# Kernel optimization log

Measured on AMD Instinct MI355X. Metric: run time of the kernel, lower is better.

## Reference

```python
import jax, jax.numpy as jnp
import numpy as np

HEADS = 16
D_MODEL = 1024
D_K = D_MODEL // HEADS


def setup_inputs() -> dict:
    key = jax.random.key(0)
    ks = jax.random.split(key, 11)
    B, S, D = 4, 2048, D_MODEL
    q = jax.random.normal(ks[0], (B, S, D), dtype=jnp.float32)
    k = jax.random.normal(ks[1], (B, S, D), dtype=jnp.float32)
    v = jax.random.normal(ks[2], (B, S, D), dtype=jnp.float32)
    s = 1.0 / np.sqrt(D)
    Wq = jax.random.normal(ks[3], (D, D), dtype=jnp.float32) * s
    bq = jax.random.normal(ks[4], (D,), dtype=jnp.float32) * 0.01
    Wk = jax.random.normal(ks[5], (D, D), dtype=jnp.float32) * s
    bk = jax.random.normal(ks[6], (D,), dtype=jnp.float32) * 0.01
    Wv = jax.random.normal(ks[7], (D, D), dtype=jnp.float32) * s
    bv = jax.random.normal(ks[8], (D,), dtype=jnp.float32) * 0.01
    Wo = jax.random.normal(ks[9], (D, D), dtype=jnp.float32) * s
    bo = jax.random.normal(ks[10], (D,), dtype=jnp.float32) * 0.01
    return {"q": q, "k": k, "v": v, "Wq": Wq, "bq": bq, "Wk": Wk, "bk": bk,
            "Wv": Wv, "bv": bv, "Wo": Wo, "bo": bo}


def reference(q, k, v, Wq, bq, Wk, bk, Wv, bv, Wo, bo):
    B, Sq, D = q.shape
    Sk = k.shape[1]
    # Linear projections (torch Linear: x @ W.T + b)
    q_ = (q @ Wq.T + bq).reshape(B, Sq, HEADS, D_K).transpose(0, 2, 1, 3)  # [B,H,Sq,Dk]
    k_ = (k @ Wk.T + bk).reshape(B, Sk, HEADS, D_K).transpose(0, 2, 1, 3)  # [B,H,Sk,Dk]
    v_ = (v @ Wv.T + bv).reshape(B, Sk, HEADS, D_K).transpose(0, 2, 1, 3)  # [B,H,Sk,Dk]
    scores = jnp.einsum("bhqd,bhkd->bhqk", q_, k_) / jnp.sqrt(jnp.float32(D_K))
    attn = jax.nn.softmax(scores, axis=-1)
    ctx = jnp.einsum("bhqk,bhkd->bhqd", attn, v_)  # [B,H,Sq,Dk]
    concat = ctx.transpose(0, 2, 1, 3).reshape(B, Sq, D)
    # dropout p=0 -> identity (eval)
    return concat @ Wo.T + bo
```

## Files before the change

kernel.cpp:

```cpp
#include <hip/hip_runtime.h>
#include <hip/hip_bf16.h>
#include <stdint.h>

typedef unsigned short u16;
typedef __attribute__((ext_vector_type(8))) short bf16x8;
typedef __attribute__((ext_vector_type(4))) float f32x4;
typedef __attribute__((ext_vector_type(16))) float f32x16;
typedef __attribute__((ext_vector_type(4))) int i32x4;
typedef __attribute__((ext_vector_type(4))) unsigned short us4;

#define BATCH 4
#define HEADS 16
#define SEQ   2048
#define DMODEL 1024
#define DK    64
#define QSCALE (0.125f * 1.44269504088896340736f)

__device__ __forceinline__ u16 f2bf(float f) {
  __hip_bfloat16 h = __float2bfloat16(f);
  return *reinterpret_cast<u16*>(&h);
}

__device__ __forceinline__ int cvtpk(float a, float b) {
  int r;
  asm("v_cvt_pk_bf16_f32 %0, %1, %2" : "=v"(r) : "v"(a), "v"(b));
  return r;
}

__device__ __forceinline__ void plswap(int& a, int& b) {
  asm volatile("v_permlane32_swap_b32 %0, %1" : "+v"(a), "+v"(b));
}

__device__ __forceinline__ void gload_lds16(const u16* g, u16* l) {
  __builtin_amdgcn_global_load_lds((const __attribute__((address_space(1))) void*)g,
                                   (__attribute__((address_space(3))) void*)l, 16, 0, 0);
}

__device__ __forceinline__ void cvt8(const float* __restrict__ in, u16* __restrict__ out, long i) {
  float4 a = *(const float4*)(in + i);
  float4 b = *(const float4*)(in + i + 4);
  i32x4 pk;
  pk[0] = cvtpk(a.x, a.y); pk[1] = cvtpk(a.z, a.w);
  pk[2] = cvtpk(b.x, b.y); pk[3] = cvtpk(b.z, b.w);
  *(i32x4*)(out + i) = pk;
}

__global__ void cvt_all(const float* __restrict__ q, const float* __restrict__ k,
                        const float* __restrict__ v, const float* __restrict__ w0,
                        const float* __restrict__ w1, const float* __restrict__ w2,
                        const float* __restrict__ w3, u16* __restrict__ qo,
                        u16* __restrict__ ko, u16* __restrict__ vo,
                        u16* __restrict__ o0, u16* __restrict__ o1,
                        u16* __restrict__ o2, u16* __restrict__ o3) {
  const int sel = blockIdx.y;
  long i = ((long)blockIdx.x * blockDim.x + threadIdx.x) * 8;
  if (sel >= 3 && i >= (long)DMODEL * DMODEL) return;
  const float* in = (sel == 0) ? q : (sel == 1) ? k : (sel == 2) ? v
                  : (sel == 3) ? w0 : (sel == 4) ? w1 : (sel == 5) ? w2 : w3;
  u16* out = (sel == 0) ? qo : (sel == 1) ? ko : (sel == 2) ? vo
           : (sel == 3) ? o0 : (sel == 4) ? o1 : (sel == 5) ? o2 : o3;
  cvt8(in, out, i);
}

__global__ __launch_bounds__(256)
void gemm_qkv(const u16* __restrict__ qb, const u16* __restrict__ kb,
              const u16* __restrict__ vb, const u16* __restrict__ Wqb,
              const u16* __restrict__ Wkb, const u16* __restrict__ Wvb,
              const float* __restrict__ bq, const float* __restrict__ bk,
              const float* __restrict__ bv, u16* __restrict__ Qp,
              u16* __restrict__ Kp, u16* __restrict__ Vt) {
  __shared__ u16 smem[128 * 64 * 2];
  u16* As = smem;
  u16* Bs = smem + 128 * 64;
  const int K = DMODEL;
  const int tid = threadIdx.x;
  const int lane = tid & 63;
  const int w = tid >> 6;
  const int wr = w >> 1, wc = w & 1;
  const int lr = lane & 15, lg = lane >> 4;

  const int wg = blockIdx.y * 24 + blockIdx.x;
  const int swz = (wg & 7) * (1536 >> 3) + (wg >> 3);
  const int bcolg = swz % 24;
  const int brow = swz / 24;
  const int sel = bcolg >> 3;
  const int bcol = bcolg & 7;

  const u16* A  = (sel == 0) ? qb : (sel == 1) ? kb : vb;
  const u16* Bm = (sel == 0) ? Wqb : (sel == 1) ? Wkb : Wvb;
  const float* bias = (sel == 0) ? bq : (sel == 1) ? bk : bv;

  const size_t aBase = (size_t)(brow * 128) * K;
  const size_t bBase = (size_t)(bcol * 128) * K;

  int srow[4], scol[4];
#pragma unroll
  for (int j = 0; j < 4; j++) {
    const int c = tid + j * 256;
    srow[j] = c >> 3;
    scol[j] = ((c & 7) ^ (srow[j] & 7)) * 8;
  }

  f32x4 acc[4][4] = {};

  for (int k0 = 0; k0 < K; k0 += 64) {
#pragma unroll
    for (int j = 0; j < 4; j++) {
      const int c = tid + j * 256;
      gload_lds16(A + aBase + (size_t)srow[j] * K + k0 + scol[j], As + c * 8);
      gload_lds16(Bm + bBase + (size_t)srow[j] * K + k0 + scol[j], Bs + c * 8);
    }
    __syncthreads();
#pragma unroll
    for (int h = 0; h < 2; h++) {
      bf16x8 a[4], b[4];
#pragma unroll
      for (int i = 0; i < 4; i++) {
        const int row = wr * 64 + i * 16 + lr;
        a[i] = *(const bf16x8*)&As[row * 64 + (((h * 4 + lg) ^ (row & 7)) * 8)];
      }
#pragma unroll
      for (int j = 0; j < 4; j++) {
        const int row = wc * 64 + j * 16 + lr;
        b[j] = *(const bf16x8*)&Bs[row * 64 + (((h * 4 + lg) ^ (row & 7)) * 8)];
      }
#pragma unroll
      for (int i = 0; i < 4; i++)
#pragma unroll
        for (int j = 0; j < 4; j++)
          acc[i][j] = __builtin_amdgcn_mfma_f32_16x16x32_bf16(a[i], b[j], acc[i][j], 0, 0, 0);
    }
    __syncthreads();
  }

  if (sel < 2) {
    u16* Cout = (sel == 0) ? Qp : Kp;
    const float oscale = (sel == 0) ? QSCALE : 1.f;
#pragma unroll
    for (int j = 0; j < 4; j++) {
      const int col = bcol * 128 + wc * 64 + j * 16 + lr;
      const float bv_ = bias[col];
#pragma unroll
      for (int i = 0; i < 4; i++) {
        const int row0 = brow * 128 + wr * 64 + i * 16 + lg * 4;
#pragma unroll
        for (int r = 0; r < 4; r++)
          Cout[(size_t)(row0 + r) * DMODEL + col] = f2bf((acc[i][j][r] + bv_) * oscale);
      }
    }
  } else {
    const int b = brow >> 4;
    const int s0 = (brow & 15) * 128;
#pragma unroll
    for (int j = 0; j < 4; j++) {
      const int col = wc * 64 + j * 16 + lr;
      const int xsw = (col & 7) << 3;
      const float bv_ = bias[bcol * 128 + col];
#pragma unroll
      for (int i = 0; i < 4; i++) {
        const int row0 = wr * 64 + i * 16 + lg * 4;
#pragma unroll
        for (int pr = 0; pr < 2; pr++) {
          float e0 = acc[i][j][pr * 2] + bv_;
          float e1 = acc[i][j][pr * 2 + 1] + bv_;
          *(int*)&smem[col * 128 + ((row0 + pr * 2) ^ xsw)] = cvtpk(e0, e1);
        }
      }
    }
    __syncthreads();
    const int col = tid >> 1, h2 = tid & 1;
    const int xsw = (col & 7) << 3;
    const int c = bcol * 128 + col;
    const int hh = c >> 6, dk = c & 63;
    u16* dst = Vt + (size_t)((b * 16 + hh) * 64 + dk) * SEQ + s0 + h2 * 64;
#pragma unroll
    for (int jj = 0; jj < 8; jj++) {
      bf16x8 vrow = *(const bf16x8*)&smem[col * 128 + ((h2 * 64 + jj * 8) ^ xsw)];
      *(bf16x8*)(dst + jj * 8) = vrow;
    }
  }
}

__global__ __launch_bounds__(256)
void gemm_bt(const u16* __restrict__ A, const u16* __restrict__ Bm,
             const float* __restrict__ bias, float* __restrict__ Cout,
             int M, int N, int K) {
  __shared__ u16 As[128 * 64];
  __shared__ u16 Bs[128 * 64];
  const int tid = threadIdx.x;
  const int lane = tid & 63;
  const int w = tid >> 6;
  const int wr = w >> 1, wc = w & 1;
  const int lr = lane & 15, lg = lane >> 4;

  const int nwg = gridDim.x * gridDim.y;
  const int wg = blockIdx.y * gridDim.x + blockIdx.x;
  const int swz = (wg & 7) * (nwg >> 3) + (wg >> 3);
  const int bcol = swz % gridDim.x;
  const int brow = swz / gridDim.x;

  const size_t aBase = (size_t)(brow * 128) * K;
  const size_t bBase = (size_t)(bcol * 128) * K;

  int srow[4], scol[4];
#pragma unroll
  for (int j = 0; j < 4; j++) {
    const int c = tid + j * 256;
    srow[j] = c >> 3;
    scol[j] = ((c & 7) ^ (srow[j] & 7)) * 8;
  }

  f32x4 acc[4][4] = {};

  for (int k0 = 0; k0 < K; k0 += 64) {
#pragma unroll
    for (int j = 0; j < 4; j++) {
      const int c = tid + j * 256;
      gload_lds16(A + aBase + (size_t)srow[j] * K + k0 + scol[j], As + c * 8);
      gload_lds16(Bm + bBase + (size_t)srow[j] * K + k0 + scol[j], Bs + c * 8);
    }
    __syncthreads();
#pragma unroll
    for (int h = 0; h < 2; h++) {
      bf16x8 a[4], b[4];
#pragma unroll
      for (int i = 0; i < 4; i++) {
        const int row = wr * 64 + i * 16 + lr;
        a[i] = *(const bf16x8*)&As[row * 64 + (((h * 4 + lg) ^ (row & 7)) * 8)];
      }
#pragma unroll
      for (int j = 0; j < 4; j++) {
        const int row = wc * 64 + j * 16 + lr;
        b[j] = *(const bf16x8*)&Bs[row * 64 + (((h * 4 + lg) ^ (row & 7)) * 8)];
      }
#pragma unroll
      for (int i = 0; i < 4; i++)
#pragma unroll
        for (int j = 0; j < 4; j++)
          acc[i][j] = __builtin_amdgcn_mfma_f32_16x16x32_bf16(a[i], b[j], acc[i][j], 0, 0, 0);
    }
    __syncthreads();
  }

#pragma unroll
  for (int j = 0; j < 4; j++) {
    const int col = bcol * 128 + wc * 64 + j * 16 + lr;
    const float bv = bias[col];
#pragma unroll
    for (int i = 0; i < 4; i++) {
      const int row0 = brow * 128 + wr * 64 + i * 16 + lg * 4;
#pragma unroll
      for (int r = 0; r < 4; r++)
        Cout[(size_t)(row0 + r) * N + col] = acc[i][j][r] + bv;
    }
  }
}

__device__ __forceinline__ void pack_group(const float* p, int* pw) {
  int W0 = cvtpk(p[0], p[1]);
  int W1 = cvtpk(p[2], p[3]);
  int W2 = cvtpk(p[4], p[5]);
  int W3 = cvtpk(p[6], p[7]);
  plswap(W0, W2);
  plswap(W1, W3);
  pw[0] = W0; pw[1] = W1; pw[2] = W2; pw[3] = W3;
}

__global__ __launch_bounds__(256, 4)
void attn2(const u16* __restrict__ Qp, const u16* __restrict__ Kp,
           const u16* __restrict__ Vt, u16* __restrict__ ctx) {
  __shared__ __align__(16) u16 smem[16384];
  const int tid = threadIdx.x;
  const int lane = tid & 63, w = tid >> 6;
  const int hi = lane >> 5;
  const int l31 = lane & 31;
  const int bh = blockIdx.y;
  const int b = bh >> 4, h = bh & 15;
  const int q0 = blockIdx.x * 128 + w * 32;

  const u16* qrow = Qp + (size_t)(b * SEQ + q0 + l31) * DMODEL + h * DK + hi * 8;
  bf16x8 qf[4];
#pragma unroll
  for (int kk = 0; kk < 4; kk++) qf[kk] = *(const bf16x8*)(qrow + kk * 16);

  const int srow = tid >> 3;
  const int scb = tid & 7;
  const int scol = (scb ^ (srow & 7)) * 8;
  const u16* kp = Kp + (size_t)(b * SEQ + srow) * DMODEL + h * DK + scol;
  const u16* vp = Vt + (size_t)bh * DK * SEQ + (size_t)srow * SEQ + scol;

  const int ksw = (l31 & 7) << 3;

  f32x16 o0 = {}, o1 = {};
  float lacc[4] = {};
  const int NT = SEQ / 64;

  {
    u16* Kd = smem;
    u16* Vd = smem + 4096;
    gload_lds16(kp, Kd + tid * 8);
    gload_lds16(kp + 32 * DMODEL, Kd + tid * 8 + 2048);
    gload_lds16(vp, Vd + tid * 8);
    gload_lds16(vp + 32 * SEQ, Vd + tid * 8 + 2048);
    kp += 64 * DMODEL;
    vp += 64;
  }
  __syncthreads();

  for (int t = 0; t < NT; ++t) {
    const int p = t & 1;
    if (t + 1 < NT) {
      u16* Kd = smem + ((p ^ 1) << 13);
      u16* Vd = Kd + 4096;
      gload_lds16(kp, Kd + tid * 8);
      gload_lds16(kp + 32 * DMODEL, Kd + tid * 8 + 2048);
      gload_lds16(vp, Vd + tid * 8);
      gload_lds16(vp + 32 * SEQ, Vd + tid * 8 + 2048);
      kp += 64 * DMODEL;
      vp += 64;
    }

    const u16* Kc = smem + (p << 13);
    const u16* Vc = Kc + 4096;

    f32x16 st0 = {}, st1 = {};
    __builtin_amdgcn_s_setprio(1);
#pragma unroll
    for (int kk = 0; kk < 4; kk++) {
      const int slot = (((kk * 2 + hi) << 3) ^ ksw);
      bf16x8 k0 = *(const bf16x8*)&Kc[l31 * 64 + slot];
      bf16x8 k1 = *(const bf16x8*)&Kc[(l31 + 32) * 64 + slot];
      st0 = __builtin_amdgcn_mfma_f32_32x32x16_bf16(k0, qf[kk], st0, 0, 0, 0);
      st1 = __builtin_amdgcn_mfma_f32_32x32x16_bf16(k1, qf[kk], st1, 0, 0, 0);
    }
    __builtin_amdgcn_s_setprio(0);

#pragma unroll
    for (int i = 0; i < 16; i++) st0[i] = __builtin_amdgcn_exp2f(st0[i]);
#pragma unroll
    for (int i = 0; i < 16; i++) st1[i] = __builtin_amdgcn_exp2f(st1[i]);
    float ts[8];
#pragma unroll
    for (int i = 0; i < 8; i++) ts[i] = (st0[i] + st0[i + 8]) + (st1[i] + st1[i + 8]);
#pragma unroll
    for (int i = 0; i < 4; i++) lacc[i] += ts[i] + ts[i + 4];

    int pw[4][4];
    {
      float tmp[8];
#pragma unroll
      for (int i = 0; i < 8; i++) tmp[i] = st0[i];
      pack_group(tmp, pw[0]);
#pragma unroll
      for (int i = 0; i < 8; i++) tmp[i] = st0[i + 8];
      pack_group(tmp, pw[1]);
#pragma unroll
      for (int i = 0; i < 8; i++) tmp[i] = st1[i];
      pack_group(tmp, pw[2]);
#pragma unroll
      for (int i = 0; i < 8; i++) tmp[i] = st1[i + 8];
      pack_group(tmp, pw[3]);
    }

    __builtin_amdgcn_s_setprio(1);
#pragma unroll
    for (int c = 0; c < 4; c++) {
      i32x4 pwv;
      pwv[0] = pw[c][0]; pwv[1] = pw[c][1]; pwv[2] = pw[c][2]; pwv[3] = pw[c][3];
      bf16x8 pf = __builtin_bit_cast(bf16x8, pwv);
      const int slot = (((c * 2 + hi) << 3) ^ ksw);
      bf16x8 v0 = *(const bf16x8*)&Vc[l31 * 64 + slot];
      bf16x8 v1 = *(const bf16x8*)&Vc[(l31 + 32) * 64 + slot];
      o0 = __builtin_amdgcn_mfma_f32_32x32x16_bf16(v0, pf, o0, 0, 0, 0);
      o1 = __builtin_amdgcn_mfma_f32_32x32x16_bf16(v1, pf, o1, 0, 0, 0);
    }
    __builtin_amdgcn_s_setprio(0);

    __syncthreads();
  }

  float lsum = (lacc[0] + lacc[1]) + (lacc[2] + lacc[3]);
  lsum += __shfl_xor(lsum, 32);
  const float rl = 1.0f / lsum;
  u16* ot = smem + w * (32 * 72);
#pragma unroll
  for (int ds_ = 0; ds_ < 2; ds_++) {
#pragma unroll
    for (int g = 0; g < 4; g++) {
#pragma unroll
      for (int pr = 0; pr < 2; pr++) {
        const int r = g * 4 + pr * 2;
        const int d = ds_ * 32 + (r & 3) + 8 * (r >> 2) + 4 * hi;
        float e0 = (ds_ ? o1[r] : o0[r]) * rl;
        float e1 = (ds_ ? o1[r + 1] : o0[r + 1]) * rl;
        *(int*)&ot[l31 * 72 + d] = cvtpk(e0, e1);
      }
    }
  }
  __syncthreads();
  const int rq = lane >> 3;
  const int rc = (lane & 7) * 8;
#pragma unroll
  for (int it = 0; it < 4; ++it) {
    const int qq = it * 8 + rq;
    bf16x8 vrow = *(const bf16x8*)&ot[qq * 72 + rc];
    *(bf16x8*)&ctx[(size_t)(b * SEQ + q0 + qq) * DMODEL + h * DK + rc] = vrow;
  }
}

extern "C" void kernel_launch(void* const* d_in, const int* in_sizes, int n_in,
                              void* d_out, int out_size, void* d_ws, size_t ws_size,
                              hipStream_t stream) {
  const float* q  = (const float*)d_in[0];
  const float* k  = (const float*)d_in[1];
  const float* v  = (const float*)d_in[2];
  const float* Wq = (const float*)d_in[3];
  const float* bq = (const float*)d_in[4];
  const float* Wk = (const float*)d_in[5];
  const float* bk = (const float*)d_in[6];
  const float* Wv = (const float*)d_in[7];
  const float* bv = (const float*)d_in[8];
  const float* Wo = (const float*)d_in[9];
  const float* bo = (const float*)d_in[10];

  char* ws = (char*)d_ws;
  const size_t MB = 1024 * 1024;
  u16* qb  = (u16*)(ws + 0 * MB);
  u16* kb  = (u16*)(ws + 16 * MB);
  u16* vb  = (u16*)(ws + 32 * MB);
  u16* Wqb = (u16*)(ws + 48 * MB);
  u16* Wkb = (u16*)(ws + 50 * MB);
  u16* Wvb = (u16*)(ws + 52 * MB);
  u16* Wob = (u16*)(ws + 54 * MB);
  u16* Qp  = (u16*)(ws + 56 * MB);
  u16* Kp  = (u16*)(ws + 72 * MB);
  u16* Vt  = (u16*)(ws + 104 * MB);
  u16* ctx = (u16*)(ws + 120 * MB);

  const long nIn = (long)BATCH * SEQ * DMODEL;

  cvt_all<<<dim3(nIn / 8 / 256, 7), 256, 0, stream>>>(q, k, v, Wq, Wk, Wv, Wo,
                                                      qb, kb, vb, Wqb, Wkb, Wvb, Wob);

  gemm_qkv<<<dim3(24, 64), 256, 0, stream>>>(qb, kb, vb, Wqb, Wkb, Wvb,
                                             bq, bk, bv, Qp, Kp, Vt);

  attn2<<<dim3(SEQ / 128, BATCH * HEADS), 256, 0, stream>>>(Qp, Kp, Vt, ctx);

  gemm_bt<<<dim3(DMODEL / 128, BATCH * SEQ / 128), 256, 0, stream>>>(
      ctx, Wob, bo, (float*)d_out, BATCH * SEQ, DMODEL, DMODEL);
}
```

Baseline: 207.1 us.

## Pipeline projection GEMMs with 256x128 tiles, multi-buffered LDS and split barriers

Replaces both projection GEMMs with a shared 512-thread, 8-wave k-loop on 256x128 tiles. A is triple-buffered and B double-buffered in LDS, with global-to-LDS prefetch issued ahead of the MFMA phases, vmcnt waits, s_setprio around the MFMA blocks and split barriers. The aim is to hide global load latency that the old load-sync-compute loop exposed and to raise reuse per tile. The attention grid also gets a workgroup swizzle for L2 locality. It relies on the larger LDS footprint and hand-placed waitcnts being correct, and grids fall to 768 and 256 blocks, which may leave some CUs idle.

```diff
diff --git a/kernel.cpp b/kernel.cpp
--- a/kernel.cpp
+++ b/kernel.cpp
@@ -7,7 +7,6 @@
 typedef __attribute__((ext_vector_type(4))) float f32x4;
 typedef __attribute__((ext_vector_type(16))) float f32x16;
 typedef __attribute__((ext_vector_type(4))) int i32x4;
-typedef __attribute__((ext_vector_type(4))) unsigned short us4;
 
 #define BATCH 4
 #define HEADS 16
@@ -35,6 +34,17 @@
   __builtin_amdgcn_global_load_lds((const __attribute__((address_space(1))) void*)g,
                                    (__attribute__((address_space(3))) void*)l, 16, 0, 0);
 }
+
+__device__ __forceinline__ void sbar() {
+  asm volatile("" ::: "memory");
+  __builtin_amdgcn_s_barrier();
+  __builtin_amdgcn_sched_barrier(0);
+}
+#define WAITV(N)                                              \
+  do {                                                        \
+    asm volatile("s_waitcnt vmcnt(" #N ")" ::: "memory");     \
+    __builtin_amdgcn_sched_barrier(0);                        \
+  } while (0)
 
 __device__ __forceinline__ void cvt8(const float* __restrict__ in, u16* __restrict__ out, long i) {
   float4 a = *(const float4*)(in + i);
@@ -62,25 +72,130 @@
   cvt8(in, out, i);
 }
 
-__global__ __launch_bounds__(256)
-void gemm_qkv(const u16* __restrict__ qb, const u16* __restrict__ kb,
-              const u16* __restrict__ vb, const u16* __restrict__ Wqb,
-              const u16* __restrict__ Wkb, const u16* __restrict__ Wvb,
-              const float* __restrict__ bq, const float* __restrict__ bk,
-              const float* __restrict__ bv, u16* __restrict__ Qp,
-              u16* __restrict__ Kp, u16* __restrict__ Vt) {
-  __shared__ u16 smem[128 * 64 * 2];
+__device__ __forceinline__ void gemm_kloop(
+    const u16* __restrict__ Ag, const u16* __restrict__ Bg,
+    u16* As, u16* Bs, f32x4 acc[4][4],
+    const int tid, const int wm, const int wn, const int lr, const int lg) {
+  const int K = DMODEL;
+  int arow[4], acolc[4], brow2[2], bcol2[2];
+#pragma unroll
+  for (int j = 0; j < 4; j++) {
+    const int c = tid + j * 512;
+    arow[j] = c >> 3;
+    acolc[j] = ((c & 7) ^ (arow[j] & 7)) * 8;
+  }
+#pragma unroll
+  for (int j = 0; j < 2; j++) {
+    const int c = tid + j * 512;
+    brow2[j] = c >> 3;
+    bcol2[j] = ((c & 7) ^ (brow2[j] & 7)) * 8;
+  }
+
+#pragma unroll
+  for (int j = 0; j < 4; j++)
+    gload_lds16(Ag + (size_t)arow[j] * K + acolc[j], As + (tid + j * 512) * 8);
+#pragma unroll
+  for (int j = 0; j < 2; j++)
+    gload_lds16(Bg + (size_t)brow2[j] * K + bcol2[j], Bs + (tid + j * 512) * 8);
+#pragma unroll
+  for (int j = 0; j < 4; j++)
+    gload_lds16(Ag + (size_t)arow[j] * K + 64 + acolc[j], As + 16384 + (tid + j * 512) * 8);
+#pragma unroll
+  for (int j = 0; j < 2; j++)
+    gload_lds16(Bg + (size_t)brow2[j] * K + 64 + bcol2[j], Bs + 8192 + (tid + j * 512) * 8);
+  WAITV(6);
+  sbar();
+
+  int m = 0;
+  for (int t = 0; t < 16; ++t) {
+    u16* Ab = As + m * 16384;
+    u16* Bb = Bs + (t & 1) * 8192;
+    const int m2 = (m + 2 >= 3) ? m - 1 : m + 2;
+    const int k1 = (t + 1) * 64;
+    const int k2 = (t + 2) * 64;
+
+    bf16x8 a[4], b[4];
+#pragma unroll
+    for (int i = 0; i < 4; i++) {
+      const int r = wm * 64 + i * 16 + lr;
+      a[i] = *(const bf16x8*)&Ab[r * 64 + ((lg ^ (r & 7)) * 8)];
+    }
+#pragma unroll
+    for (int j = 0; j < 4; j++) {
+      const int r = wn * 64 + j * 16 + lr;
+      b[j] = *(const bf16x8*)&Bb[r * 64 + ((lg ^ (r & 7)) * 8)];
+    }
+    if (t + 1 < 16) {
+      u16* Bd = Bs + ((t + 1) & 1) * 8192;
+      gload_lds16(Bg + (size_t)brow2[0] * K + k1 + bcol2[0], Bd + tid * 8);
+      gload_lds16(Bg + (size_t)brow2[1] * K + k1 + bcol2[1], Bd + (tid + 512) * 8);
+    }
+    if (t + 2 < 16) {
+      u16* Ad = As + m2 * 16384;
+      gload_lds16(Ag + (size_t)arow[0] * K + k2 + acolc[0], Ad + tid * 8);
+      gload_lds16(Ag + (size_t)arow[1] * K + k2 + acolc[1], Ad + (tid + 512) * 8);
+    }
+    sbar();
+    __builtin_amdgcn_s_setprio(1);
+#pragma unroll
+    for (int i = 0; i < 4; i++)
+#pragma unroll
+      for (int j = 0; j < 4; j++)
+        acc[i][j] = __builtin_amdgcn_mfma_f32_16x16x32_bf16(a[i], b[j], acc[i][j], 0, 0, 0);
+    __builtin_amdgcn_s_setprio(0);
+    sbar();
+
+#pragma unroll
+    for (int i = 0; i < 4; i++) {
+      const int r = wm * 64 + i * 16 + lr;
+      a[i] = *(const bf16x8*)&Ab[r * 64 + (((4 + lg) ^ (r & 7)) * 8)];
+    }
+#pragma unroll
+    for (int j = 0; j < 4; j++) {
+      const int r = wn * 64 + j * 16 + lr;
+      b[j] = *(const bf16x8*)&Bb[r * 64 + (((4 + lg) ^ (r & 7)) * 8)];
+    }
+    if (t + 2 < 16) {
+      u16* Ad = As + m2 * 16384;
+      gload_lds16(Ag + (size_t)arow[2] * K + k2 + acolc[2], Ad + (tid + 1024) * 8);
+      gload_lds16(Ag + (size_t)arow[3] * K + k2 + acolc[3], Ad + (tid + 1536) * 8);
+    }
+    sbar();
+    __builtin_amdgcn_s_setprio(1);
+#pragma unroll
+    for (int i = 0; i < 4; i++)
+#pragma unroll
+      for (int j = 0; j < 4; j++)
+        acc[i][j] = __builtin_amdgcn_mfma_f32_16x16x32_bf16(a[i], b[j], acc[i][j], 0, 0, 0);
+    __builtin_amdgcn_s_setprio(0);
+    if (t < 14) {
+      WAITV(4);
+    } else {
+      WAITV(0);
+    }
+    sbar();
+    m = (m + 1 >= 3) ? 0 : m + 1;
+  }
+}
+
+__global__ __launch_bounds__(512, 2)
+void gemm8_qkv(const u16* __restrict__ qb, const u16* __restrict__ kb,
+               const u16* __restrict__ vb, const u16* __restrict__ Wqb,
+               const u16* __restrict__ Wkb, const u16* __restrict__ Wvb,
+               const float* __restrict__ bq, const float* __restrict__ bk,
+               const float* __restrict__ bv, u16* __restrict__ Qp,
+               u16* __restrict__ Kp, u16* __restrict__ Vt) {
+  __shared__ __align__(16) u16 smem[65536];
   u16* As = smem;
-  u16* Bs = smem + 128 * 64;
-  const int K = DMODEL;
+  u16* Bs = smem + 49152;
   const int tid = threadIdx.x;
   const int lane = tid & 63;
   const int w = tid >> 6;
-  const int wr = w >> 1, wc = w & 1;
+  const int wm = w >> 1, wn = w & 1;
   const int lr = lane & 15, lg = lane >> 4;
 
   const int wg = blockIdx.y * 24 + blockIdx.x;
-  const int swz = (wg & 7) * (1536 >> 3) + (wg >> 3);
+  const int swz = (wg & 7) * 96 + (wg >> 3);
   const int bcolg = swz % 24;
   const int brow = swz / 24;
   const int sel = bcolg >> 3;
@@ -90,168 +205,92 @@
   const u16* Bm = (sel == 0) ? Wqb : (sel == 1) ? Wkb : Wvb;
   const float* bias = (sel == 0) ? bq : (sel == 1) ? bk : bv;
 
-  const size_t aBase = (size_t)(brow * 128) * K;
-  const size_t bBase = (size_t)(bcol * 128) * K;
-
-  int srow[4], scol[4];
-#pragma unroll
-  for (int j = 0; j < 4; j++) {
-    const int c = tid + j * 256;
-    srow[j] = c >> 3;
-    scol[j] = ((c & 7) ^ (srow[j] & 7)) * 8;
-  }
-
   f32x4 acc[4][4] = {};
-
-  for (int k0 = 0; k0 < K; k0 += 64) {
-#pragma unroll
-    for (int j = 0; j < 4; j++) {
-      const int c = tid + j * 256;
-      gload_lds16(A + aBase + (size_t)srow[j] * K + k0 + scol[j], As + c * 8);
-      gload_lds16(Bm + bBase + (size_t)srow[j] * K + k0 + scol[j], Bs + c * 8);
-    }
-    __syncthreads();
-#pragma unroll
-    for (int h = 0; h < 2; h++) {
-      bf16x8 a[4], b[4];
-#pragma unroll
-      for (int i = 0; i < 4; i++) {
-        const int row = wr * 64 + i * 16 + lr;
-        a[i] = *(const bf16x8*)&As[row * 64 + (((h * 4 + lg) ^ (row & 7)) * 8)];
-      }
-#pragma unroll
-      for (int j = 0; j < 4; j++) {
-        const int row = wc * 64 + j * 16 + lr;
-        b[j] = *(const bf16x8*)&Bs[row * 64 + (((h * 4 + lg) ^ (row & 7)) * 8)];
-      }
-#pragma unroll
-      for (int i = 0; i < 4; i++)
-#pragma unroll
-        for (int j = 0; j < 4; j++)
-          acc[i][j] = __builtin_amdgcn_mfma_f32_16x16x32_bf16(a[i], b[j], acc[i][j], 0, 0, 0);
-    }
-    __syncthreads();
-  }
+  gemm_kloop(A + (size_t)(brow * 256) * DMODEL, Bm + (size_t)(bcol * 128) * DMODEL,
+             As, Bs, acc, tid, wm, wn, lr, lg);
 
   if (sel < 2) {
     u16* Cout = (sel == 0) ? Qp : Kp;
     const float oscale = (sel == 0) ? QSCALE : 1.f;
 #pragma unroll
     for (int j = 0; j < 4; j++) {
-      const int col = bcol * 128 + wc * 64 + j * 16 + lr;
+      const int col = bcol * 128 + wn * 64 + j * 16 + lr;
       const float bv_ = bias[col];
 #pragma unroll
       for (int i = 0; i < 4; i++) {
-        const int row0 = brow * 128 + wr * 64 + i * 16 + lg * 4;
+        const int row0 = brow * 256 + wm * 64 + i * 16 + lg * 4;
 #pragma unroll
         for (int r = 0; r < 4; r++)
           Cout[(size_t)(row0 + r) * DMODEL + col] = f2bf((acc[i][j][r] + bv_) * oscale);
       }
     }
   } else {
-    const int b = brow >> 4;
-    const int s0 = (brow & 15) * 128;
+    const int b = brow >> 3;
+    const int s0 = (brow & 7) * 256;
+    u16* tr = smem;
+    __syncthreads();
 #pragma unroll
     for (int j = 0; j < 4; j++) {
-      const int col = wc * 64 + j * 16 + lr;
+      const int col = wn * 64 + j * 16 + lr;
       const int xsw = (col & 7) << 3;
       const float bv_ = bias[bcol * 128 + col];
 #pragma unroll
       for (int i = 0; i < 4; i++) {
-        const int row0 = wr * 64 + i * 16 + lg * 4;
+        const int r0 = wm * 64 + i * 16 + lg * 4;
 #pragma unroll
         for (int pr = 0; pr < 2; pr++) {
-          float e0 = acc[i][j][pr * 2] + bv_;
-          float e1 = acc[i][j][pr * 2 + 1] + bv_;
-          *(int*)&smem[col * 128 + ((row0 + pr * 2) ^ xsw)] = cvtpk(e0, e1);
+          const float e0 = acc[i][j][pr * 2] + bv_;
+          const float e1 = acc[i][j][pr * 2 + 1] + bv_;
+          *(int*)&tr[col * 256 + ((r0 + pr * 2) ^ xsw)] = cvtpk(e0, e1);
         }
       }
     }
     __syncthreads();
-    const int col = tid >> 1, h2 = tid & 1;
+    const int col = tid >> 2;
+    const int part = tid & 3;
     const int xsw = (col & 7) << 3;
     const int c = bcol * 128 + col;
     const int hh = c >> 6, dk = c & 63;
-    u16* dst = Vt + (size_t)((b * 16 + hh) * 64 + dk) * SEQ + s0 + h2 * 64;
+    u16* dst = Vt + (size_t)((b * 16 + hh) * 64 + dk) * SEQ + s0 + part * 64;
 #pragma unroll
     for (int jj = 0; jj < 8; jj++) {
-      bf16x8 vrow = *(const bf16x8*)&smem[col * 128 + ((h2 * 64 + jj * 8) ^ xsw)];
-      *(bf16x8*)(dst + jj * 8) = vrow;
-    }
-  }
-}
-
-__global__ __launch_bounds__(256)
-void gemm_bt(const u16* __restrict__ A, const u16* __restrict__ Bm,
-             const float* __restrict__ bias, float* __restrict__ Cout,
-             int M, int N, int K) {
-  __shared__ u16 As[128 * 64];
-  __shared__ u16 Bs[128 * 64];
+      bf16x8 vv = *(const bf16x8*)&tr[col * 256 + ((part * 64 + jj * 8) ^ xsw)];
+      *(bf16x8*)(dst + jj * 8) = vv;
+    }
+  }
+}
+
+__global__ __launch_bounds__(512, 2)
+void gemm8_bt(const u16* __restrict__ A, const u16* __restrict__ Bm,
+              const float* __restrict__ bias, float* __restrict__ Cout) {
+  __shared__ __align__(16) u16 smem[65536];
+  u16* As = smem;
+  u16* Bs = smem + 49152;
   const int tid = threadIdx.x;
   const int lane = tid & 63;
   const int w = tid >> 6;
-  const int wr = w >> 1, wc = w & 1;
+  const int wm = w >> 1, wn = w & 1;
   const int lr = lane & 15, lg = lane >> 4;
 
-  const int nwg = gridDim.x * gridDim.y;
-  const int wg = blockIdx.y * gridDim.x + blockIdx.x;
-  const int swz = (wg & 7) * (nwg >> 3) + (wg >> 3);
-  const int bcol = swz % gridDim.x;
-  const int brow = swz / gridDim.x;
-
-  const size_t aBase = (size_t)(brow * 128) * K;
-  const size_t bBase = (size_t)(bcol * 128) * K;
-
-  int srow[4], scol[4];
+  const int wg = blockIdx.y * 8 + blockIdx.x;
+  const int swz = (wg & 7) * 32 + (wg >> 3);
+  const int bcol = swz & 7;
+  const int brow = swz >> 3;
+
+  f32x4 acc[4][4] = {};
+  gemm_kloop(A + (size_t)(brow * 256) * DMODEL, Bm + (size_t)(bcol * 128) * DMODEL,
+             As, Bs, acc, tid, wm, wn, lr, lg);
+
 #pragma unroll
   for (int j = 0; j < 4; j++) {
-    const int c = tid + j * 256;
-    srow[j] = c >> 3;
-    scol[j] = ((c & 7) ^ (srow[j] & 7)) * 8;
-  }
-
-  f32x4 acc[4][4] = {};
-
-  for (int k0 = 0; k0 < K; k0 += 64) {
-#pragma unroll
-    for (int j = 0; j < 4; j++) {
-      const int c = tid + j * 256;
-      gload_lds16(A + aBase + (size_t)srow[j] * K + k0 + scol[j], As + c * 8);
-      gload_lds16(Bm + bBase + (size_t)srow[j] * K + k0 + scol[j], Bs + c * 8);
-    }
-    __syncthreads();
-#pragma unroll
-    for (int h = 0; h < 2; h++) {
-      bf16x8 a[4], b[4];
-#pragma unroll
-      for (int i = 0; i < 4; i++) {
-        const int row = wr * 64 + i * 16 + lr;
-        a[i] = *(const bf16x8*)&As[row * 64 + (((h * 4 + lg) ^ (row & 7)) * 8)];
-      }
-#pragma unroll
-      for (int j = 0; j < 4; j++) {
-        const int row = wc * 64 + j * 16 + lr;
-        b[j] = *(const bf16x8*)&Bs[row * 64 + (((h * 4 + lg) ^ (row & 7)) * 8)];
-      }
-#pragma unroll
-      for (int i = 0; i < 4; i++)
-#pragma unroll
-        for (int j = 0; j < 4; j++)
-          acc[i][j] = __builtin_amdgcn_mfma_f32_16x16x32_bf16(a[i], b[j], acc[i][j], 0, 0, 0);
-    }
-    __syncthreads();
-  }
-
-#pragma unroll
-  for (int j = 0; j < 4; j++) {
-    const int col = bcol * 128 + wc * 64 + j * 16 + lr;
-    const float bv = bias[col];
+    const int col = bcol * 128 + wn * 64 + j * 16 + lr;
+    const float bv_ = bias[col];
 #pragma unroll
     for (int i = 0; i < 4; i++) {
-      const int row0 = brow * 128 + wr * 64 + i * 16 + lg * 4;
+      const int row0 = brow * 256 + wm * 64 + i * 16 + lg * 4;
 #pragma unroll
       for (int r = 0; r < 4; r++)
-        Cout[(size_t)(row0 + r) * N + col] = acc[i][j][r] + bv;
+        Cout[(size_t)(row0 + r) * DMODEL + col] = acc[i][j][r] + bv_;
     }
   }
 }
@@ -274,9 +313,12 @@
   const int lane = tid & 63, w = tid >> 6;
   const int hi = lane >> 5;
   const int l31 = lane & 31;
-  const int bh = blockIdx.y;
+
+  const int wg = blockIdx.y * gridDim.x + blockIdx.x;
+  const int swz = (wg & 7) * 128 + (wg >> 3);
+  const int bh = swz >> 4;
   const int b = bh >> 4, h = bh & 15;
-  const int q0 = blockIdx.x * 128 + w * 32;
+  const int q0 = (swz & 15) * 128 + w * 32;
 
   const u16* qrow = Qp + (size_t)(b * SEQ + q0 + l31) * DMODEL + h * DK + hi * 8;
   bf16x8 qf[4];
@@ -442,11 +484,10 @@
   cvt_all<<<dim3(nIn / 8 / 256, 7), 256, 0, stream>>>(q, k, v, Wq, Wk, Wv, Wo,
                                                       qb, kb, vb, Wqb, Wkb, Wvb, Wob);
 
-  gemm_qkv<<<dim3(24, 64), 256, 0, stream>>>(qb, kb, vb, Wqb, Wkb, Wvb,
-                                             bq, bk, bv, Qp, Kp, Vt);
-
-  attn2<<<dim3(SEQ / 128, BATCH * HEADS), 256, 0, stream>>>(Qp, Kp, Vt, ctx);
-
-  gemm_bt<<<dim3(DMODEL / 128, BATCH * SEQ / 128), 256, 0, stream>>>(
-      ctx, Wob, bo, (float*)d_out, BATCH * SEQ, DMODEL, DMODEL);
-}
+  gemm8_qkv<<<dim3(24, 32), 512, 0, stream>>>(qb, kb, vb, Wqb, Wkb, Wvb,
+                                              bq, bk, bv, Qp, Kp, Vt);
+
+  attn2<<<dim3(16, 64), 256, 0, stream>>>(Qp, Kp, Vt, ctx);
+
+  gemm8_bt<<<dim3(8, 32), 512, 0, stream>>>(ctx, Wob, bo, (float*)d_out);
+}
```

Measured after the change: 198.8 us. 4.0% less time.
